# Kernel tuning notes

Measured on AMD Instinct MI355X. Metric: run time of the kernel, lower is better.

Reference implementation:

```python
import jax, jax.numpy as jnp
import numpy as np

jax.config.update("jax_enable_x64", True)  # original does TPS solve in float64

GRID_SIZE = 5
NUM_POINTS = GRID_SIZE * GRID_SIZE
EPS = 1e-6


def _initial_control_points():
    cp = np.linspace(-1.0, 1.0, GRID_SIZE)
    p, q = np.meshgrid(cp, cp, indexing='ij')
    return jnp.asarray(np.stack([p.ravel(), q.ravel()], axis=1), dtype=jnp.float32)


def setup_inputs() -> dict:
    key = jax.random.key(0)
    k1, k2, k3 = jax.random.split(key, 3)
    B, C, H, W = 8, 64, 256, 256
    t = jax.random.normal(k1, (B, C, H, W), dtype=jnp.float32)
    rgb = jax.random.normal(k2, (B, C, H, W), dtype=jnp.float32)
    fc_w = jax.random.normal(k3, (NUM_POINTS * 2, 2 * C), dtype=jnp.float32) * 0.01
    fc_b = jnp.zeros((NUM_POINTS * 2,), dtype=jnp.float32)
    init_cp = _initial_control_points()
    return {"t": t, "rgb": rgb, "fc_w": fc_w, "fc_b": fc_b, "init_cp": init_cp}


def _tps_grid(cp, init_cp, out_h, out_w):
    # cp: [B,N,2] f64 target control points; init_cp: [N,2] f64 source points
    B, N, _ = cp.shape
    P = init_cp
    # TPS kernel on source control points (identical across batch)
    d2 = jnp.sum((P[:, None, :] - P[None, :, :]) ** 2, axis=-1)            # [N,N]
    K = d2 * jnp.log(d2 + EPS)
    P_aug = jnp.concatenate([jnp.ones((N, 1), cp.dtype), P], axis=1)       # [N,3]
    L = jnp.zeros((N + 3, N + 3), cp.dtype)
    L = L.at[:N, :N].set(K).at[:N, N:].set(P_aug).at[N:, :N].set(P_aug.T)
    Y = jnp.concatenate([cp, jnp.zeros((B, 3, 2), cp.dtype)], axis=1)      # [B,N+3,2]
    Wm = jnp.einsum('ij,bjc->bic', jnp.linalg.pinv(L), Y)                  # [B,N+3,2]
    # Evaluate TPS on dense grid (x varies slowest, matching torch meshgrid 'ij')
    gx = jnp.linspace(-1.0, 1.0, out_w, dtype=cp.dtype)
    gy = jnp.linspace(-1.0, 1.0, out_h, dtype=cp.dtype)
    gp, gq = jnp.meshgrid(gx, gy, indexing='ij')
    g = jnp.stack([gp.ravel(), gq.ravel()], axis=1)                        # [out_w*out_h, 2]
    d2g = jnp.sum((g[:, None, :] - P[None, :, :]) ** 2, axis=-1)           # [M,N]
    U = d2g * jnp.log(d2g + EPS)
    g_aug = jnp.concatenate([U, jnp.ones((g.shape[0], 1), cp.dtype), g], axis=1)  # [M,N+3]
    grid = jnp.einsum('mk,bkc->bmc', g_aug, Wm)                            # [B,M,2]
    grid = grid.reshape(B, out_w, out_h, 2).transpose(0, 2, 1, 3)          # [B,H,W,2]
    return grid.astype(jnp.float32)


def _grid_sample(img, grid):
    # bilinear, padding_mode='border', align_corners=True
    B, C, H, W = img.shape
    x = jnp.clip((grid[..., 0] + 1.0) * 0.5 * (W - 1), 0.0, W - 1)         # [B,Ho,Wo]
    y = jnp.clip((grid[..., 1] + 1.0) * 0.5 * (H - 1), 0.0, H - 1)
    x0f, y0f = jnp.floor(x), jnp.floor(y)
    x0 = x0f.astype(jnp.int32)
    y0 = y0f.astype(jnp.int32)
    x1 = jnp.clip(x0 + 1, 0, W - 1)
    y1 = jnp.clip(y0 + 1, 0, H - 1)
    wx = (x - x0f)[:, None]                                                # [B,1,Ho,Wo]
    wy = (y - y0f)[:, None]

    def gather(xi, yi):
        return jax.vmap(lambda im, yy, xx: im[:, yy, xx])(img, yi, xi)     # [B,C,Ho,Wo]

    v00 = gather(x0, y0)
    v01 = gather(x1, y0)
    v10 = gather(x0, y1)
    v11 = gather(x1, y1)
    top = v00 * (1.0 - wx) + v01 * wx
    bot = v10 * (1.0 - wx) + v11 * wx
    return top * (1.0 - wy) + bot * wy


def reference(t, rgb, fc_w, fc_b, init_cp):
    B = t.shape[0]
    feat = jnp.concatenate([t, rgb], axis=1).mean(axis=(2, 3))             # adaptive avg pool to 1x1
    delta = (feat @ fc_w.T + fc_b).reshape(B, NUM_POINTS, 2)
    cp = init_cp[None] + delta                                             # [B,N,2]
    grid = _tps_grid(cp.astype(jnp.float64), init_cp.astype(jnp.float64), t.shape[2], t.shape[3])
    out = _grid_sample(t, grid)
    return out, cp
```

## Files before the change

kernel.cpp:

```cpp
#include <hip/hip_runtime.h>
#include <hip/hip_bf16.h>

#define B_  8
#define C_  64
#define H_  256
#define W_  256
#define HW_ (H_ * W_)
#define NP_ 25
#define NA_ 28
#define NRHS_ 16
#define NCOL_ (NA_ + NRHS_)
#define PARTS_ 8
#define CHUNK_ (HW_ / PARTS_)

__global__ __launch_bounds__(256) void mean_partial_kernel(const float* __restrict__ t,
                                                           const float* __restrict__ rgb,
                                                           float* __restrict__ partial) {
    int blk  = blockIdx.x;
    bool is_t = blk >= 4096;
    int idx  = (is_t ? blk - 4096 : blk) >> 3;
    int part = blk & 7;
    int b    = idx >> 6;
    int cloc = idx & 63;
    int chan = b * 128 + (is_t ? cloc : 64 + cloc);

    const float* src = (is_t ? t : rgb) + ((size_t)(b * C_ + cloc)) * HW_ + part * CHUNK_;
    const float4* s4 = (const float4*)src;

    float s = 0.f;
    int base = threadIdx.x;
    #pragma unroll
    for (int i = 0; i < CHUNK_ / 4 / 256; ++i) {
        float4 v = s4[base + i * 256];
        s += (v.x + v.y) + (v.z + v.w);
    }
    #pragma unroll
    for (int off = 32; off > 0; off >>= 1) s += __shfl_down(s, off);
    __shared__ float red[4];
    if ((threadIdx.x & 63) == 0) red[threadIdx.x >> 6] = s;
    __syncthreads();
    if (threadIdx.x == 0)
        partial[chan * PARTS_ + part] = (red[0] + red[1]) + (red[2] + red[3]);
}

__global__ __launch_bounds__(256) void solve_kernel(const float* __restrict__ partial,
                                                    const float* __restrict__ fc_w,
                                                    const float* __restrict__ fc_b,
                                                    const float* __restrict__ init_cp,
                                                    float* __restrict__ cp_out,
                                                    double* __restrict__ Wm) {
    __shared__ float  s_feat[B_ * 128];
    __shared__ float  s_cp[B_][2 * NP_];
    __shared__ double P[NP_][2];
    __shared__ double A[NA_][NCOL_];
    __shared__ double f[NA_];
    __shared__ int    s_piv;
    __shared__ double s_pv;
    int tid = threadIdx.x;

    for (int i = tid; i < B_ * 128; i += 256) {
        const float* p = partial + i * PARTS_;
        float s = 0.f;
        #pragma unroll
        for (int j = 0; j < PARTS_; ++j) s += p[j];
        s_feat[i] = s * (1.0f / (float)HW_);
    }
    if (tid < 2 * NP_) ((double*)P)[tid] = (double)init_cp[tid];
    __syncthreads();

    for (int i = tid; i < B_ * 2 * NP_; i += 256) {
        int b = i / (2 * NP_), j = i % (2 * NP_);
        float acc = fc_b[j];
        const float* w  = fc_w + j * 128;
        const float* fe = s_feat + b * 128;
        #pragma unroll 8
        for (int c = 0; c < 128; ++c) acc += fe[c] * w[c];
        float cpv = init_cp[j] + acc;
        s_cp[b][j] = cpv;
        cp_out[b * 2 * NP_ + j] = cpv;
    }
    __syncthreads();

    for (int i = tid; i < NA_ * NCOL_; i += 256) {
        int r = i / NCOL_, cc = i % NCOL_;
        double v;
        if (cc < NA_) {
            if (r < NP_ && cc < NP_) {
                double dx = P[r][0] - P[cc][0];
                double dy = P[r][1] - P[cc][1];
                double d2 = dx * dx + dy * dy;
                v = d2 * log(d2 + 1e-6);
            } else if (r < NP_) {
                v = (cc == NP_) ? 1.0 : ((cc == NP_ + 1) ? P[r][0] : P[r][1]);
            } else if (cc < NP_) {
                v = (r == NP_) ? 1.0 : ((r == NP_ + 1) ? P[cc][0] : P[cc][1]);
            } else {
                v = 0.0;
            }
        } else {
            int y = cc - NA_;
            int b = y >> 1, k = y & 1;
            v = (r < NP_) ? (double)s_cp[b][r * 2 + k] : 0.0;
        }
        A[r][cc] = v;
    }
    __syncthreads();

    for (int k = 0; k < NA_; ++k) {
        if (tid == 0) {
            int piv = k; double best = fabs(A[k][k]);
            for (int r = k + 1; r < NA_; ++r) {
                double v = fabs(A[r][k]);
                if (v > best) { best = v; piv = r; }
            }
            s_piv = piv;
        }
        __syncthreads();
        int piv = s_piv;
        if (piv != k) {
            for (int j = tid; j < NCOL_; j += 256) {
                double tmp = A[k][j]; A[k][j] = A[piv][j]; A[piv][j] = tmp;
            }
        }
        __syncthreads();
        if (tid == 0) s_pv = 1.0 / A[k][k];
        __syncthreads();
        double pv = s_pv;
        for (int j = tid; j < NCOL_; j += 256) A[k][j] *= pv;
        __syncthreads();
        if (tid < NA_) f[tid] = A[tid][k];
        __syncthreads();
        for (int i = tid; i < NA_ * NCOL_; i += 256) {
            int r = i / NCOL_, j = i % NCOL_;
            if (r != k) A[r][j] -= f[r] * A[k][j];
        }
        __syncthreads();
    }

    for (int i = tid; i < B_ * NA_ * 2; i += 256) {
        int b = i / (NA_ * 2), rest = i % (NA_ * 2);
        int n = rest >> 1, c = rest & 1;
        Wm[i] = A[n][NA_ + b * 2 + c];
    }
}

__global__ __launch_bounds__(256) void sample_kernel(const float* __restrict__ t,
                                                     const float* __restrict__ init_cp,
                                                     const double* __restrict__ Wm,
                                                     float* __restrict__ out) {
    int blk = blockIdx.x;
    int b = blk >> 8;
    int y = blk & 255;
    int x = threadIdx.x;

    __shared__ float sW[NA_][2];
    __shared__ float sP[NP_][2];
    if (x < 2 * NA_)
        ((float*)sW)[x] = (float)Wm[(size_t)b * 2 * NA_ + x];
    else if (x < 2 * NA_ + 2 * NP_)
        ((float*)sP)[x - 2 * NA_] = init_cp[x - 2 * NA_];
    __syncthreads();

    float px = -1.0f + (2.0f / (float)(W_ - 1)) * (float)x;
    float py = -1.0f + (2.0f / (float)(H_ - 1)) * (float)y;

    float ax = sW[NP_][0] + px * sW[NP_ + 1][0] + py * sW[NP_ + 2][0];
    float ay = sW[NP_][1] + px * sW[NP_ + 1][1] + py * sW[NP_ + 2][1];
    #pragma unroll
    for (int n = 0; n < NP_; ++n) {
        float dx = px - sP[n][0];
        float dy = py - sP[n][1];
        float d2 = dx * dx + dy * dy;
        float u  = d2 * logf(d2 + 1e-6f);
        ax += u * sW[n][0];
        ay += u * sW[n][1];
    }

    float xf = fminf(fmaxf((ax + 1.0f) * 0.5f * (float)(W_ - 1), 0.0f), (float)(W_ - 1));
    float yf = fminf(fmaxf((ay + 1.0f) * 0.5f * (float)(H_ - 1), 0.0f), (float)(H_ - 1));
    float x0f = floorf(xf), y0f = floorf(yf);
    int x0 = (int)x0f, y0 = (int)y0f;
    int x1 = min(x0 + 1, W_ - 1);
    int y1 = min(y0 + 1, H_ - 1);
    float wx = xf - x0f, wy = yf - y0f;
    float omwx = 1.0f - wx, omwy = 1.0f - wy;

    int i00 = y0 * W_ + x0;
    int i01 = y0 * W_ + x1;
    int i10 = y1 * W_ + x0;
    int i11 = y1 * W_ + x1;

    const float* tb = t   + (size_t)b * C_ * HW_;
    float*       ob = out + (size_t)b * C_ * HW_ + y * W_ + x;
    #pragma unroll 4
    for (int c = 0; c < C_; ++c) {
        const float* tc = tb + (size_t)c * HW_;
        float top = tc[i00] * omwx + tc[i01] * wx;
        float bot = tc[i10] * omwx + tc[i11] * wx;
        ob[(size_t)c * HW_] = top * omwy + bot * wy;
    }
}

extern "C" void kernel_launch(void* const* d_in, const int* in_sizes, int n_in,
                              void* d_out, int out_size, void* d_ws, size_t ws_size,
                              hipStream_t stream) {
    const float* t       = (const float*)d_in[0];
    const float* rgb     = (const float*)d_in[1];
    const float* fc_w    = (const float*)d_in[2];
    const float* fc_b    = (const float*)d_in[3];
    const float* init_cp = (const float*)d_in[4];

    float* out    = (float*)d_out;
    float* cp_out = out + (size_t)B_ * C_ * HW_;

    float*  partial = (float*)d_ws;
    double* Wm      = (double*)((char*)d_ws + 32768);

    mean_partial_kernel<<<B_ * 2 * C_ * PARTS_, 256, 0, stream>>>(t, rgb, partial);
    solve_kernel<<<1, 256, 0, stream>>>(partial, fc_w, fc_b, init_cp, cp_out, Wm);
    sample_kernel<<<B_ * H_, 256, 0, stream>>>(t, init_cp, Wm, out);
}
```

Baseline: 173.9 us.

## Fuse mean, per-batch TPS solve and sampling into one persistent ticketed kernel

Result: slower. 536.8 us (+208.7%).

```diff
diff --git a/kernel.cpp b/kernel.cpp
--- a/kernel.cpp
+++ b/kernel.cpp
@@ -8,196 +8,229 @@
 #define HW_ (H_ * W_)
 #define NP_ 25
 #define NA_ 28
-#define NRHS_ 16
-#define NCOL_ (NA_ + NRHS_)
-#define PARTS_ 8
-#define CHUNK_ (HW_ / PARTS_)
-
-__global__ __launch_bounds__(256) void mean_partial_kernel(const float* __restrict__ t,
-                                                           const float* __restrict__ rgb,
-                                                           float* __restrict__ partial) {
-    int blk  = blockIdx.x;
-    bool is_t = blk >= 4096;
-    int idx  = (is_t ? blk - 4096 : blk) >> 3;
-    int part = blk & 7;
-    int b    = idx >> 6;
-    int cloc = idx & 63;
-    int chan = b * 128 + (is_t ? cloc : 64 + cloc);
-
-    const float* src = (is_t ? t : rgb) + ((size_t)(b * C_ + cloc)) * HW_ + part * CHUNK_;
-    const float4* s4 = (const float4*)src;
-
-    float s = 0.f;
-    int base = threadIdx.x;
-    #pragma unroll
-    for (int i = 0; i < CHUNK_ / 4 / 256; ++i) {
-        float4 v = s4[base + i * 256];
-        s += (v.x + v.y) + (v.z + v.w);
-    }
-    #pragma unroll
-    for (int off = 32; off > 0; off >>= 1) s += __shfl_down(s, off);
-    __shared__ float red[4];
-    if ((threadIdx.x & 63) == 0) red[threadIdx.x >> 6] = s;
-    __syncthreads();
-    if (threadIdx.x == 0)
-        partial[chan * PARTS_ + part] = (red[0] + red[1]) + (red[2] + red[3]);
-}
-
-__global__ __launch_bounds__(256) void solve_kernel(const float* __restrict__ partial,
+#define NCOLS_ 30
+
+#define TK_MEAN_END  2048
+#define TK_SOLVE_END 2056
+#define TK_TOTAL     4104
+
+#define F_TICKET 0
+#define F_MEAND  8
+#define F_SOLVED 16
+
+typedef float f32x4 __attribute__((ext_vector_type(4)));
+
+__global__ __launch_bounds__(256) void fused_kernel(const float* __restrict__ t,
+                                                    const float* __restrict__ rgb,
                                                     const float* __restrict__ fc_w,
                                                     const float* __restrict__ fc_b,
                                                     const float* __restrict__ init_cp,
+                                                    float* __restrict__ out,
                                                     float* __restrict__ cp_out,
+                                                    int* __restrict__ flags,
+                                                    float* __restrict__ feat_part,
                                                     double* __restrict__ Wm) {
-    __shared__ float  s_feat[B_ * 128];
-    __shared__ float  s_cp[B_][2 * NP_];
-    __shared__ double P[NP_][2];
-    __shared__ double A[NA_][NCOL_];
-    __shared__ double f[NA_];
-    __shared__ int    s_piv;
-    __shared__ double s_pv;
+    __shared__ int s_ticket;
     int tid = threadIdx.x;
 
-    for (int i = tid; i < B_ * 128; i += 256) {
-        const float* p = partial + i * PARTS_;
-        float s = 0.f;
-        #pragma unroll
-        for (int j = 0; j < PARTS_; ++j) s += p[j];
-        s_feat[i] = s * (1.0f / (float)HW_);
-    }
-    if (tid < 2 * NP_) ((double*)P)[tid] = (double)init_cp[tid];
-    __syncthreads();
-
-    for (int i = tid; i < B_ * 2 * NP_; i += 256) {
-        int b = i / (2 * NP_), j = i % (2 * NP_);
-        float acc = fc_b[j];
-        const float* w  = fc_w + j * 128;
-        const float* fe = s_feat + b * 128;
-        #pragma unroll 8
-        for (int c = 0; c < 128; ++c) acc += fe[c] * w[c];
-        float cpv = init_cp[j] + acc;
-        s_cp[b][j] = cpv;
-        cp_out[b * 2 * NP_ + j] = cpv;
-    }
-    __syncthreads();
-
-    for (int i = tid; i < NA_ * NCOL_; i += 256) {
-        int r = i / NCOL_, cc = i % NCOL_;
-        double v;
-        if (cc < NA_) {
-            if (r < NP_ && cc < NP_) {
-                double dx = P[r][0] - P[cc][0];
-                double dy = P[r][1] - P[cc][1];
-                double d2 = dx * dx + dy * dy;
-                v = d2 * log(d2 + 1e-6);
-            } else if (r < NP_) {
-                v = (cc == NP_) ? 1.0 : ((cc == NP_ + 1) ? P[r][0] : P[r][1]);
-            } else if (cc < NP_) {
-                v = (r == NP_) ? 1.0 : ((r == NP_ + 1) ? P[cc][0] : P[cc][1]);
+    for (;;) {
+        if (tid == 0)
+            s_ticket = __hip_atomic_fetch_add(&flags[F_TICKET], 1,
+                                              __ATOMIC_RELAXED, __HIP_MEMORY_SCOPE_AGENT);
+        __syncthreads();
+        int tk = s_ticket;
+        if (tk >= TK_TOTAL) return;
+
+        if (tk < TK_MEAN_END) {
+            int b = tk >> 8;
+            int c = (tk >> 1) & 127;
+            int h = tk & 1;
+            bool is_rgb = (c >= C_);
+            const float* base = (is_rgb ? rgb + ((size_t)(b * C_ + (c - C_))) * HW_
+                                        : t   + ((size_t)(b * C_ + c)) * HW_)
+                                + h * (HW_ / 2);
+            const f32x4* s4 = (const f32x4*)base;
+            float acc = 0.f;
+            if (is_rgb) {
+                #pragma unroll 4
+                for (int k = 0; k < 32; ++k) {
+                    f32x4 v = __builtin_nontemporal_load(s4 + tid + k * 256);
+                    acc += (v.x + v.y) + (v.z + v.w);
+                }
             } else {
-                v = 0.0;
+                #pragma unroll 4
+                for (int k = 0; k < 32; ++k) {
+                    f32x4 v = s4[tid + k * 256];
+                    acc += (v.x + v.y) + (v.z + v.w);
+                }
+            }
+            #pragma unroll
+            for (int off = 32; off > 0; off >>= 1) acc += __shfl_down(acc, off);
+            __shared__ float red[4];
+            if ((tid & 63) == 0) red[tid >> 6] = acc;
+            __syncthreads();
+            if (tid == 0) {
+                float tot = (red[0] + red[1]) + (red[2] + red[3]);
+                feat_part[b * 256 + c * 2 + h] = tot * (1.0f / 65536.0f);
+                __threadfence();
+                __hip_atomic_fetch_add(&flags[F_MEAND + b], 1,
+                                       __ATOMIC_RELEASE, __HIP_MEMORY_SCOPE_AGENT);
+            }
+        } else if (tk < TK_SOLVE_END) {
+            int b = tk - TK_MEAN_END;
+            if (tid == 0) {
+                while (__hip_atomic_load(&flags[F_MEAND + b],
+                                         __ATOMIC_ACQUIRE, __HIP_MEMORY_SCOPE_AGENT) < 256) {
+                    __builtin_amdgcn_s_sleep(7);
+                    __builtin_amdgcn_s_sleep(7);
+                }
+            }
+            __syncthreads();
+
+            __shared__ float  s_cp2[2 * NP_];
+            __shared__ double Pd[2 * NP_];
+            __shared__ double A[NA_][NCOLS_];
+            __shared__ double fcol[NA_];
+            __shared__ int    s_piv;
+            __shared__ double s_pv;
+
+            if (tid < 2 * NP_) {
+                float accv = fc_b[tid];
+                const float* fp = feat_part + b * 256;
+                const float* w  = fc_w + tid * 128;
+                #pragma unroll 8
+                for (int c2 = 0; c2 < 128; ++c2)
+                    accv += (fp[2 * c2] + fp[2 * c2 + 1]) * w[c2];
+                float cpv = init_cp[tid] + accv;
+                s_cp2[tid] = cpv;
+                cp_out[b * 2 * NP_ + tid] = cpv;
+                Pd[tid] = (double)init_cp[tid];
+            }
+            __syncthreads();
+
+            for (int i = tid; i < NA_ * NCOLS_; i += 256) {
+                int r = i / NCOLS_, cc = i % NCOLS_;
+                double v;
+                if (cc < NA_) {
+                    if (r < NP_ && cc < NP_) {
+                        double dx = Pd[r * 2] - Pd[cc * 2];
+                        double dy = Pd[r * 2 + 1] - Pd[cc * 2 + 1];
+                        double d2 = dx * dx + dy * dy;
+                        v = d2 * log(d2 + 1e-6);
+                    } else if (r < NP_) {
+                        v = (cc == NP_) ? 1.0 : ((cc == NP_ + 1) ? Pd[r * 2] : Pd[r * 2 + 1]);
+                    } else if (cc < NP_) {
+                        v = (r == NP_) ? 1.0 : ((r == NP_ + 1) ? Pd[cc * 2] : Pd[cc * 2 + 1]);
+                    } else {
+                        v = 0.0;
+                    }
+                } else {
+                    v = (r < NP_) ? (double)s_cp2[r * 2 + (cc - NA_)] : 0.0;
+                }
+                A[r][cc] = v;
+            }
+            __syncthreads();
+
+            for (int k = 0; k < NA_; ++k) {
+                if (tid == 0) {
+                    int piv = k; double best = fabs(A[k][k]);
+                    for (int r = k + 1; r < NA_; ++r) {
+                        double v = fabs(A[r][k]);
+                        if (v > best) { best = v; piv = r; }
+                    }
+                    s_piv = piv;
+                }
+                __syncthreads();
+                int piv = s_piv;
+                if (piv != k && tid < NCOLS_) {
+                    double tmp = A[k][tid]; A[k][tid] = A[piv][tid]; A[piv][tid] = tmp;
+                }
+                __syncthreads();
+                if (tid == 0) s_pv = 1.0 / A[k][k];
+                __syncthreads();
+                if (tid < NCOLS_) A[k][tid] *= s_pv;
+                __syncthreads();
+                if (tid < NA_) fcol[tid] = A[tid][k];
+                __syncthreads();
+                for (int i = tid; i < NA_ * NCOLS_; i += 256) {
+                    int r = i / NCOLS_, j = i % NCOLS_;
+                    if (r != k) A[r][j] -= fcol[r] * A[k][j];
+                }
+                __syncthreads();
+            }
+
+            if (tid < NA_ * 2) {
+                int n = tid >> 1, k2 = tid & 1;
+                Wm[b * (NA_ * 2) + n * 2 + k2] = A[n][NA_ + k2];
+            }
+            __syncthreads();
+            if (tid == 0) {
+                __threadfence();
+                __hip_atomic_store(&flags[F_SOLVED + b], 1,
+                                   __ATOMIC_RELEASE, __HIP_MEMORY_SCOPE_AGENT);
             }
         } else {
-            int y = cc - NA_;
-            int b = y >> 1, k = y & 1;
-            v = (r < NP_) ? (double)s_cp[b][r * 2 + k] : 0.0;
-        }
-        A[r][cc] = v;
-    }
-    __syncthreads();
-
-    for (int k = 0; k < NA_; ++k) {
-        if (tid == 0) {
-            int piv = k; double best = fabs(A[k][k]);
-            for (int r = k + 1; r < NA_; ++r) {
-                double v = fabs(A[r][k]);
-                if (v > best) { best = v; piv = r; }
-            }
-            s_piv = piv;
+            int u  = tk - TK_SOLVE_END;
+            int sb = u >> 8;
+            int y  = u & 255;
+            if (tid == 0) {
+                while (!__hip_atomic_load(&flags[F_SOLVED + sb],
+                                          __ATOMIC_ACQUIRE, __HIP_MEMORY_SCOPE_AGENT)) {
+                    for (int j = 0; j < 8; ++j) __builtin_amdgcn_s_sleep(7);
+                }
+            }
+            __syncthreads();
+
+            __shared__ float sW[NA_][2];
+            __shared__ float sP2[NP_][2];
+            if (tid < 2 * NA_)
+                ((float*)sW)[tid] = (float)Wm[sb * (NA_ * 2) + tid];
+            else if (tid < 2 * NA_ + 2 * NP_)
+                ((float*)sP2)[tid - 2 * NA_] = init_cp[tid - 2 * NA_];
+            __syncthreads();
+
+            int x = tid;
+            float px = -1.0f + (2.0f / (float)(W_ - 1)) * (float)x;
+            float py = -1.0f + (2.0f / (float)(H_ - 1)) * (float)y;
+
+            float ax = sW[NP_][0] + px * sW[NP_ + 1][0] + py * sW[NP_ + 2][0];
+            float ay = sW[NP_][1] + px * sW[NP_ + 1][1] + py * sW[NP_ + 2][1];
+            #pragma unroll
+            for (int n = 0; n < NP_; ++n) {
+                float dx = px - sP2[n][0];
+                float dy = py - sP2[n][1];
+                float d2 = dx * dx + dy * dy;
+                float ub = d2 * logf(d2 + 1e-6f);
+                ax += ub * sW[n][0];
+                ay += ub * sW[n][1];
+            }
+
+            float xf = fminf(fmaxf((ax + 1.0f) * 0.5f * (float)(W_ - 1), 0.0f), (float)(W_ - 1));
+            float yf = fminf(fmaxf((ay + 1.0f) * 0.5f * (float)(H_ - 1), 0.0f), (float)(H_ - 1));
+            float x0f = floorf(xf), y0f = floorf(yf);
+            int x0 = (int)x0f, y0 = (int)y0f;
+            int x1 = min(x0 + 1, W_ - 1);
+            int y1 = min(y0 + 1, H_ - 1);
+            float wx = xf - x0f, wy = yf - y0f;
+            float omwx = 1.0f - wx, omwy = 1.0f - wy;
+
+            int i00 = y0 * W_ + x0;
+            int i01 = y0 * W_ + x1;
+            int i10 = y1 * W_ + x0;
+            int i11 = y1 * W_ + x1;
+
+            const float* tb = t   + (size_t)sb * C_ * HW_;
+            float*       ob = out + (size_t)sb * C_ * HW_ + y * W_ + x;
+            #pragma unroll 4
+            for (int c = 0; c < C_; ++c) {
+                const float* tc = tb + (size_t)c * HW_;
+                float top = tc[i00] * omwx + tc[i01] * wx;
+                float bot = tc[i10] * omwx + tc[i11] * wx;
+                float v = top * omwy + bot * wy;
+                __builtin_nontemporal_store(v, ob + (size_t)c * HW_);
+            }
         }
         __syncthreads();
-        int piv = s_piv;
-        if (piv != k) {
-            for (int j = tid; j < NCOL_; j += 256) {
-                double tmp = A[k][j]; A[k][j] = A[piv][j]; A[piv][j] = tmp;
-            }
-        }
-        __syncthreads();
-        if (tid == 0) s_pv = 1.0 / A[k][k];
-        __syncthreads();
-        double pv = s_pv;
-        for (int j = tid; j < NCOL_; j += 256) A[k][j] *= pv;
-        __syncthreads();
-        if (tid < NA_) f[tid] = A[tid][k];
-        __syncthreads();
-        for (int i = tid; i < NA_ * NCOL_; i += 256) {
-            int r = i / NCOL_, j = i % NCOL_;
-            if (r != k) A[r][j] -= f[r] * A[k][j];
-        }
-        __syncthreads();
-    }
-
-    for (int i = tid; i < B_ * NA_ * 2; i += 256) {
-        int b = i / (NA_ * 2), rest = i % (NA_ * 2);
-        int n = rest >> 1, c = rest & 1;
-        Wm[i] = A[n][NA_ + b * 2 + c];
-    }
-}
-
-__global__ __launch_bounds__(256) void sample_kernel(const float* __restrict__ t,
-                                                     const float* __restrict__ init_cp,
-                                                     const double* __restrict__ Wm,
-                                                     float* __restrict__ out) {
-    int blk = blockIdx.x;
-    int b = blk >> 8;
-    int y = blk & 255;
-    int x = threadIdx.x;
-
-    __shared__ float sW[NA_][2];
-    __shared__ float sP[NP_][2];
-    if (x < 2 * NA_)
-        ((float*)sW)[x] = (float)Wm[(size_t)b * 2 * NA_ + x];
-    else if (x < 2 * NA_ + 2 * NP_)
-        ((float*)sP)[x - 2 * NA_] = init_cp[x - 2 * NA_];
-    __syncthreads();
-
-    float px = -1.0f + (2.0f / (float)(W_ - 1)) * (float)x;
-    float py = -1.0f + (2.0f / (float)(H_ - 1)) * (float)y;
-
-    float ax = sW[NP_][0] + px * sW[NP_ + 1][0] + py * sW[NP_ + 2][0];
-    float ay = sW[NP_][1] + px * sW[NP_ + 1][1] + py * sW[NP_ + 2][1];
-    #pragma unroll
-    for (int n = 0; n < NP_; ++n) {
-        float dx = px - sP[n][0];
-        float dy = py - sP[n][1];
-        float d2 = dx * dx + dy * dy;
-        float u  = d2 * logf(d2 + 1e-6f);
-        ax += u * sW[n][0];
-        ay += u * sW[n][1];
-    }
-
-    float xf = fminf(fmaxf((ax + 1.0f) * 0.5f * (float)(W_ - 1), 0.0f), (float)(W_ - 1));
-    float yf = fminf(fmaxf((ay + 1.0f) * 0.5f * (float)(H_ - 1), 0.0f), (float)(H_ - 1));
-    float x0f = floorf(xf), y0f = floorf(yf);
-    int x0 = (int)x0f, y0 = (int)y0f;
-    int x1 = min(x0 + 1, W_ - 1);
-    int y1 = min(y0 + 1, H_ - 1);
-    float wx = xf - x0f, wy = yf - y0f;
-    float omwx = 1.0f - wx, omwy = 1.0f - wy;
-
-    int i00 = y0 * W_ + x0;
-    int i01 = y0 * W_ + x1;
-    int i10 = y1 * W_ + x0;
-    int i11 = y1 * W_ + x1;
-
-    const float* tb = t   + (size_t)b * C_ * HW_;
-    float*       ob = out + (size_t)b * C_ * HW_ + y * W_ + x;
-    #pragma unroll 4
-    for (int c = 0; c < C_; ++c) {
-        const float* tc = tb + (size_t)c * HW_;
-        float top = tc[i00] * omwx + tc[i01] * wx;
-        float bot = tc[i10] * omwx + tc[i11] * wx;
-        ob[(size_t)c * HW_] = top * omwy + bot * wy;
     }
 }
 
@@ -213,10 +246,11 @@
     float* out    = (float*)d_out;
     float* cp_out = out + (size_t)B_ * C_ * HW_;
 
-    float*  partial = (float*)d_ws;
-    double* Wm      = (double*)((char*)d_ws + 32768);
-
-    mean_partial_kernel<<<B_ * 2 * C_ * PARTS_, 256, 0, stream>>>(t, rgb, partial);
-    solve_kernel<<<1, 256, 0, stream>>>(partial, fc_w, fc_b, init_cp, cp_out, Wm);
-    sample_kernel<<<B_ * H_, 256, 0, stream>>>(t, init_cp, Wm, out);
+    int*    flags     = (int*)d_ws;
+    float*  feat_part = (float*)((char*)d_ws + 1024);
+    double* Wm        = (double*)((char*)d_ws + 16384);
+
+    hipMemsetAsync(d_ws, 0, 256, stream);
+    fused_kernel<<<2048, 256, 0, stream>>>(t, rgb, fc_w, fc_b, init_cp,
+                                           out, cp_out, flags, feat_part, Wm);
 }
```
